# Optimization experiments

Hardware: AMD Instinct MI355X
Metric: run time of the kernel (lower is better)

Reference implementation:

```python
import jax, jax.numpy as jnp
import numpy as np


def _cayley():
    # Cl(3,0) basis blades ordered by grade, lexicographic: 1,e1,e2,e3,e12,e13,e23,e123
    blades = [0b000, 0b001, 0b010, 0b100, 0b011, 0b101, 0b110, 0b111]
    idx = {b: i for i, b in enumerate(blades)}
    C = np.zeros((8, 8, 8), np.float32)
    for a in blades:
        for b in blades:
            t, s = a >> 1, 0
            while t:
                s += bin(t & b).count('1')
                t >>= 1
            C[idx[a], idx[a ^ b], idx[b]] = -1.0 if (s & 1) else 1.0
    return jnp.asarray(C)

CAYLEY = _cayley()                      # [8,8,8], metric [1,1,1]
GRADE = jnp.array([0, 1, 1, 1, 2, 2, 2, 3])  # blade -> grade (subspace) index
N_NODES, N_EDGES = 5, 20
NUM_HEADS = 8


def mv_linear(x, w, b):
    # MVLinear with subspaces=True: one scalar weight per (out, in, grade),
    # expanded to the 8 blades; bias only on the grade-0 (scalar) blade.
    # x: [N, m, 8], w: [n, m, 4], b: [n]
    out = jnp.einsum('bmi,nmi->bni', x, w[:, :, GRADE])
    return out.at[..., 0].add(b)


def _ln(x, g, b):
    m = jnp.mean(x, axis=-1, keepdims=True)
    v = jnp.var(x, axis=-1, keepdims=True)
    return (x - m) * jax.lax.rsqrt(v + 1e-5) * g + b


def _forward(nodes, edges, src_mask, batch_size, W_in, b_in, W_gp, b_gp,
             Wq, Wk, Wv, Wo, ln1_g, ln1_b, ln2_g, ln2_b, W1, b1, W2, b2):
    B = batch_size
    S = N_NODES + N_EDGES
    c_in = nodes.shape[1]
    nodes4 = nodes.reshape(B, N_NODES, c_in, 8)
    edges4 = edges.reshape(B, N_EDGES, c_in, 8)
    src = jnp.concatenate([nodes4, edges4], axis=1).reshape(B * S, c_in, 8)

    src_mv = mv_linear(src, W_in, b_in)                               # [B*S, dm, 8]
    src_gp = jnp.einsum('bni,ijk,bnk->bnj', src_mv, CAYLEY, src_mv)   # geometric product
    src2 = mv_linear(jnp.concatenate([src_mv, src_gp], axis=1), W_gp, b_gp)

    dm = src2.shape[1]
    D = dm * 8                                                        # 56 flat features
    H = NUM_HEADS
    hd = D // H
    x = src2.reshape(B, S, D)

    L = Wq.shape[0]
    for l in range(L):                                                # fixed small layer count
        h = _ln(x, ln1_g[l], ln1_b[l])
        q = (h @ Wq[l]).reshape(B, S, H, hd)
        k = (h @ Wk[l]).reshape(B, S, H, hd)
        v = (h @ Wv[l]).reshape(B, S, H, hd)
        scores = jnp.einsum('bqhd,bkhd->bhqk', q, k) / jnp.sqrt(jnp.float32(hd))
        scores = scores + src_mask[:, None, :, :]
        attn = jax.nn.softmax(scores, axis=-1)
        o = jnp.einsum('bhqk,bkhd->bqhd', attn, v).reshape(B, S, D)
        x = x + o @ Wo[l]
        h2 = _ln(x, ln2_g[l], ln2_b[l])
        x = x + jax.nn.gelu(h2 @ W1[l] + b1[l]) @ W2[l] + b2[l]

    out = x.reshape(B, S, dm, 8)
    sel = out[:, :N_NODES, 1, :]                                      # feature channel 1
    return sel.reshape(B * N_NODES, 8)


def setup_inputs() -> dict:
    key = jax.random.key(0)
    ks = jax.random.split(key, 12)
    B, c_in, dm, L = 4096, 3, 7, 4
    D = dm * 8
    Dff = 4 * D

    def r(k, shp, s=0.02):
        return jax.random.normal(k, shp, jnp.float32) * s

    return dict(
        nodes=jax.random.normal(ks[0], (B * N_NODES, c_in, 8), jnp.float32),
        edges=jax.random.normal(ks[1], (B * N_EDGES, c_in, 8), jnp.float32),
        src_mask=jnp.zeros((B, 25, 25), jnp.float32),
        batch_size=B,
        W_in=r(ks[2], (dm, c_in, 4), 1.0 / np.sqrt(c_in)),
        b_in=jnp.zeros((dm,), jnp.float32),
        W_gp=r(ks[3], (dm, 2 * dm, 4), 1.0 / np.sqrt(2 * dm)),
        b_gp=jnp.zeros((dm,), jnp.float32),
        Wq=r(ks[4], (L, D, D)), Wk=r(ks[5], (L, D, D)),
        Wv=r(ks[6], (L, D, D)), Wo=r(ks[7], (L, D, D)),
        ln1_g=jnp.ones((L, D), jnp.float32), ln1_b=jnp.zeros((L, D), jnp.float32),
        ln2_g=jnp.ones((L, D), jnp.float32), ln2_b=jnp.zeros((L, D), jnp.float32),
        W1=r(ks[8], (L, D, Dff)), b1=jnp.zeros((L, Dff), jnp.float32),
        W2=r(ks[9], (L, Dff, D)), b2=jnp.zeros((L, D), jnp.float32),
    )


def reference(nodes, edges, src_mask, batch_size, W_in, b_in, W_gp, b_gp,
              Wq, Wk, Wv, Wo, ln1_g, ln1_b, ln2_g, ln2_b, W1, b1, W2, b2):
    return _forward(nodes, edges, src_mask, batch_size, W_in, b_in, W_gp, b_gp,
                    Wq, Wk, Wv, Wo, ln1_g, ln1_b, ln2_g, ln2_b, W1, b1, W2, b2)
```

## Files before the change

kernel.cpp:

```cpp
#include <hip/hip_runtime.h>
#include <math.h>

#define NTH 256
#define XSTR 56
#define QHSTR 72
#define FSTR 224
#define LOG2E 1.4426950408889634f

typedef __attribute__((ext_vector_type(8))) short short8;
typedef __attribute__((ext_vector_type(4))) float f32x4;
typedef _Float16 half2_t __attribute__((ext_vector_type(2)));

__device__ __forceinline__ half2_t as_h2(unsigned int u) {
    return __builtin_bit_cast(half2_t, u);
}
__device__ __forceinline__ float fast_exp2(float x) {
    float r;
    asm("v_exp_f32 %0, %1" : "=v"(r) : "v"(x));
    return r;
}
__device__ __forceinline__ unsigned short f2bf(float x) {
    unsigned int u = __float_as_uint(x);
    return (unsigned short)((u + 0x7FFFu + ((u >> 16) & 1u)) >> 16);
}
__device__ __forceinline__ unsigned short f2bf_t(float x) {
    return (unsigned short)(__float_as_uint(x) >> 16);
}

__host__ __device__ constexpr int pc_(int v) { int c = 0; while (v) { c += v & 1; v >>= 1; } return c; }
__host__ __device__ constexpr int gp_sign(int a, int b) {
    int s = 0; int t = a >> 1;
    while (t) { s += pc_(t & b); t >>= 1; }
    return (s & 1) ? -1 : 1;
}
#define BLADE(i) ((int)((0x76534210u >> ((i) * 4)) & 0xF))

__device__ __forceinline__ float gelu_sig(float z) {
    float E = fast_exp2(-2.4554669f * z);
    return z * __builtin_amdgcn_rcpf(1.0f + E);
}

__global__ void prep_weights(const float* __restrict__ Wq, const float* __restrict__ Wk,
                             const float* __restrict__ Wv, const float* __restrict__ Wo,
                             const float* __restrict__ W1, const float* __restrict__ W2,
                             unsigned short* __restrict__ ws, int L)
{
    int idx = blockIdx.x * NTH + threadIdx.x;
    int total1 = L * 16384, total2 = L * 14336, total3 = L * 14336;
    if (idx < total1) {
        int k = idx & 63, n = (idx >> 6) & 63, mat = (idx >> 12) & 3, l = idx >> 14;
        float v = 0.f;
        if (k < 56 && n < 56) {
            const float* W = (mat == 0) ? Wq : (mat == 1) ? Wk : (mat == 2) ? Wv : Wo;
            v = W[l * 3136 + k * 56 + n];
            if (mat == 0) v *= 0.3779644730092272f * LOG2E;
        }
        ws[idx] = f2bf(v);
    } else if (idx < total1 + total2) {
        int t = idx - total1;
        int k = t & 63, n = (t >> 6) % 224, l = t / 14336;
        float v = (k < 56) ? W1[l * 12544 + k * 224 + n] : 0.f;
        ws[idx] = f2bf(v);
    } else if (idx < total1 + total2 + total3) {
        int t = idx - total1 - total2;
        int k = t % 224, n = (t / 224) & 63, l = t / 14336;
        float v = (n < 56) ? W2[l * 12544 + k * 56 + n] : 0.f;
        ws[idx] = f2bf(v);
    }
}

__global__ __launch_bounds__(NTH, 4) void nbody_fused(
    const float* __restrict__ nodes, const float* __restrict__ edges,
    const float* __restrict__ src_mask,
    const float* __restrict__ W_in, const float* __restrict__ b_in,
    const float* __restrict__ W_gp, const float* __restrict__ b_gp,
    const float* __restrict__ ln1g, const float* __restrict__ ln1b,
    const float* __restrict__ ln2g, const float* __restrict__ ln2b,
    const float* __restrict__ b1, const float* __restrict__ b2,
    const unsigned short* __restrict__ ws, int L, int Btot,
    float* __restrict__ out)
{
    __shared__ __align__(16) float XS[2][25 * XSTR];
    __shared__ __align__(16) unsigned short HB[2][1800];
    __shared__ __align__(16) unsigned short UNI[2][5600];

    const int b0 = blockIdx.x * 2, tid = threadIdx.x;
    const int lane = tid & 63, wid = tid >> 6;
    const int nl = lane & 15, quad = lane >> 4;
    const int col = wid * 16 + nl;
    const int pcolh = (col / 7) * 8 + col % 7;
    const int ln_g = lane >> 3, ln_p = lane & 7;
    const int ln_s = wid + 4 * ln_g;
    int rA1 = 16 + nl; if (rA1 > 24) rA1 = 24;
    const int bbm1 = (b0 + 1 < Btot) ? (b0 + 1) : (Btot - 1);

    for (int t = tid; t < 1200; t += NTH) {
        int ss = t / 600, r0 = t - ss * 600;
        int s = r0 / 24, r = r0 % 24;
        int bb = b0 + ss;
        if (bb < Btot)
            XS[ss][r0] = (s < 5) ? nodes[bb * 120 + r0] : edges[bb * 480 + (s - 5) * 24 + r];
    }
    for (int t = tid; t < 400; t += NTH) {
        int ss = t / 200, r0 = t - ss * 200;
        int r = r0 >> 3, c = 56 + (r0 & 7);
        HB[ss][r * 72 + c] = 0;
    }
    __syncthreads();

    #pragma unroll
    for (int ss = 0; ss < 2; ss++) {
        const float* SRCF = XS[ss];
        float* KBs = (float*)UNI[ss];
        for (int t = tid; t < 1400; t += NTH) {
            int s = t / 56, rem = t % 56, n = rem >> 3, i = rem & 7;
            int g = __popc(BLADE(i));
            float acc = (i == 0) ? b_in[n] : 0.0f;
            #pragma unroll
            for (int m = 0; m < 3; m++)
                acc += SRCF[s * 24 + m * 8 + i] * W_in[n * 12 + m * 4 + g];
            KBs[s * 56 + rem] = acc;
        }
    }
    __syncthreads();

    #pragma unroll
    for (int ss = 0; ss < 2; ss++) {
        float* KBs = (float*)UNI[ss];
        float* VBs = KBs + 1400;
        for (int t = tid; t < 175; t += NTH) {
            int s = t / 7, n = t % 7;
            float m8[8], g8[8];
            #pragma unroll
            for (int i = 0; i < 8; i++) { m8[i] = KBs[s * 56 + n * 8 + i]; g8[i] = 0.0f; }
            #pragma unroll
            for (int ai = 0; ai < 8; ai++) {
                const int a = BLADE(ai);
                #pragma unroll
                for (int bi = 0; bi < 8; bi++) {
                    const int bb = BLADE(bi);
                    const int j = BLADE(a ^ bb);
                    const int sg = gp_sign(a, bb);
                    g8[j] += (sg > 0) ? (m8[ai] * m8[bi]) : (-m8[ai] * m8[bi]);
                }
            }
            #pragma unroll
            for (int j = 0; j < 8; j++) VBs[s * 56 + n * 8 + j] = g8[j];
        }
    }
    __syncthreads();

    #pragma unroll
    for (int ss = 0; ss < 2; ss++) {
        const float* KBs = (const float*)UNI[ss];
        const float* VBs = KBs + 1400;
        for (int t = tid; t < 1400; t += NTH) {
            int s = t / 56, rem = t % 56, n = rem >> 3, i = rem & 7;
            int g = __popc(BLADE(i));
            float acc = (i == 0) ? b_gp[n] : 0.0f;
            #pragma unroll
            for (int m = 0; m < 7; m++)
                acc += KBs[s * 56 + m * 8 + i] * W_gp[n * 56 + m * 4 + g];
            #pragma unroll
            for (int m = 0; m < 7; m++)
                acc += VBs[s * 56 + m * 8 + i] * W_gp[n * 56 + (7 + m) * 4 + g];
            XS[ss][s * XSTR + rem] = acc;
        }
    }
    __syncthreads();

    const unsigned short* w1t_all = ws + (size_t)L * 16384;
    const unsigned short* w2t_all = w1t_all + (size_t)L * 14336;

    for (int l = 0; l < L; l++) {
        const float* g1 = ln1g + l * 56; const float* e1 = ln1b + l * 56;
        const float* g2 = ln2g + l * 56; const float* e2 = ln2b + l * 56;

        if (tid < 200) {
            int s = tid >> 3, hh = tid & 7;
            #pragma unroll
            for (int ss = 0; ss < 2; ss++) {
                _Float16* QH = (_Float16*)UNI[ss];
                _Float16* KH = QH + 25 * QHSTR;
                QH[s * QHSTR + hh * 8 + 7] = (_Float16)0.f;
                KH[s * QHSTR + hh * 8 + 7] = (_Float16)0.f;
            }
        }
        #pragma unroll
        for (int ss = 0; ss < 2; ss++) {
            float x[7]; float sum = 0.f, sq = 0.f;
            if (ln_s < 25) {
                const float* xp = XS[ss] + ln_s * XSTR + ln_p * 7;
                #pragma unroll
                for (int j = 0; j < 7; j++) { x[j] = xp[j]; sum += x[j]; sq += x[j] * x[j]; }
            }
            #pragma unroll
            for (int off = 1; off < 8; off <<= 1) {
                sum += __shfl_xor(sum, off, 64);
                sq  += __shfl_xor(sq,  off, 64);
            }
            if (ln_s < 25) {
                float mean = sum * (1.0f / 56.0f);
                float rs = __builtin_amdgcn_rsqf(sq * (1.0f / 56.0f) - mean * mean + 1e-5f);
                unsigned short* hp = HB[ss] + ln_s * 72 + ln_p * 7;
                #pragma unroll
                for (int j = 0; j < 7; j++) {
                    int d = ln_p * 7 + j;
                    hp[j] = f2bf_t((x[j] - mean) * rs * g1[d] + e1[d]);
                }
            }
        }
        __syncthreads();

        {
            short8 a[2][2][2];
            #pragma unroll
            for (int ss = 0; ss < 2; ss++)
                #pragma unroll
                for (int ks = 0; ks < 2; ks++) {
                    a[ss][0][ks] = *(const short8*)(HB[ss] + nl * 72 + ks * 32 + quad * 8);
                    a[ss][1][ks] = *(const short8*)(HB[ss] + rA1 * 72 + ks * 32 + quad * 8);
                }
            #pragma unroll
            for (int mat = 0; mat < 3; mat++) {
                const unsigned short* bp = ws + (((size_t)(l * 4 + mat)) << 12) + (((size_t)col) << 6) + quad * 8;
                short8 b0f = *(const short8*)(bp);
                short8 b1f = *(const short8*)(bp + 32);
                #pragma unroll
                for (int ss = 0; ss < 2; ss++) {
                    f32x4 acc0 = {0, 0, 0, 0}, acc1 = {0, 0, 0, 0};
                    acc0 = __builtin_amdgcn_mfma_f32_16x16x32_bf16(a[ss][0][0], b0f, acc0, 0, 0, 0);
                    acc0 = __builtin_amdgcn_mfma_f32_16x16x32_bf16(a[ss][0][1], b1f, acc0, 0, 0, 0);
                    acc1 = __builtin_amdgcn_mfma_f32_16x16x32_bf16(a[ss][1][0], b0f, acc1, 0, 0, 0);
                    acc1 = __builtin_amdgcn_mfma_f32_16x16x32_bf16(a[ss][1][1], b1f, acc1, 0, 0, 0);
                    _Float16* dst = (_Float16*)UNI[ss] + mat * 25 * QHSTR;
                    if (col < 56) {
                        #pragma unroll
                        for (int r = 0; r < 4; r++) {
                            int row0 = quad * 4 + r;
                            dst[row0 * QHSTR + pcolh] = (_Float16)acc0[r];
                            int row1 = 16 + row0;
                            if (row1 < 25) dst[row1 * QHSTR + pcolh] = (_Float16)acc1[r];
                        }
                    }
                }
            }
        }
        __syncthreads();

        if (tid < 200) {
            int s = tid >> 3, hh = tid & 7;
            const _Float16* QHa = (const _Float16*)UNI[0];
            const _Float16* QHb = (const _Float16*)UNI[1];
            const _Float16* KHa = QHa + 25 * QHSTR, * VHa = KHa + 25 * QHSTR;
            const _Float16* KHb = QHb + 25 * QHSTR, * VHb = KHb + 25 * QHSTR;
            const float* mka = src_mask + (size_t)b0 * 625 + s * 25;
            const float* mkb = src_mask + (size_t)bbm1 * 625 + s * 25;
            uint4 Qa = *(const uint4*)(QHa + s * QHSTR + hh * 8);
            uint4 Qb = *(const uint4*)(QHb + s * QHSTR + hh * 8);
            half2_t qa0 = as_h2(Qa.x), qa1 = as_h2(Qa.y), qa2 = as_h2(Qa.z), qa3 = as_h2(Qa.w);
            half2_t qb0 = as_h2(Qb.x), qb1 = as_h2(Qb.y), qb2 = as_h2(Qb.z), qb3 = as_h2(Qb.w);
            float lsa = 0.f, lsb = 0.f;
            half2_t aa0 = {0,0}, aa1 = {0,0}, aa2 = {0,0}, aa3 = {0,0};
            half2_t ab0 = {0,0}, ab1 = {0,0}, ab2 = {0,0}, ab3 = {0,0};
            for (int kk = 0; kk < 25; kk++) {
                uint4 Ka = *(const uint4*)(KHa + kk * QHSTR + hh * 8);
                uint4 Kb = *(const uint4*)(KHb + kk * QHSTR + hh * 8);
                float da = mka[kk] * LOG2E;
                float db = mkb[kk] * LOG2E;
                da = __builtin_amdgcn_fdot2(qa3, as_h2(Ka.w), da, false);
                db = __builtin_amdgcn_fdot2(qb3, as_h2(Kb.w), db, false);
                da = __builtin_amdgcn_fdot2(qa2, as_h2(Ka.z), da, false);
                db = __builtin_amdgcn_fdot2(qb2, as_h2(Kb.z), db, false);
                da = __builtin_amdgcn_fdot2(qa1, as_h2(Ka.y), da, false);
                db = __builtin_amdgcn_fdot2(qb1, as_h2(Kb.y), db, false);
                da = __builtin_amdgcn_fdot2(qa0, as_h2(Ka.x), da, false);
                db = __builtin_amdgcn_fdot2(qb0, as_h2(Kb.x), db, false);
                float pa = fast_exp2(da);
                float pb = fast_exp2(db);
                lsa += pa; lsb += pb;
                uint4 Va = *(const uint4*)(VHa + kk * QHSTR + hh * 8);
                uint4 Vb = *(const uint4*)(VHb + kk * QHSTR + hh * 8);
                _Float16 pha = (_Float16)pa, phb = (_Float16)pb;
                half2_t p2a = {pha, pha}, p2b = {phb, phb};
                aa0 += p2a * as_h2(Va.x); aa1 += p2a * as_h2(Va.y);
                aa2 += p2a * as_h2(Va.z); aa3 += p2a * as_h2(Va.w);
                ab0 += p2b * as_h2(Vb.x); ab1 += p2b * as_h2(Vb.y);
                ab2 += p2b * as_h2(Vb.z); ab3 += p2b * as_h2(Vb.w);
            }
            float inva = __builtin_amdgcn_rcpf(lsa);
            float invb = __builtin_amdgcn_rcpf(lsb);
            unsigned short* opa = HB[0] + s * 72 + hh * 7;
            unsigned short* opb = HB[1] + s * 72 + hh * 7;
            opa[0] = f2bf_t((float)aa0.x * inva); opa[1] = f2bf_t((float)aa0.y * inva);
            opa[2] = f2bf_t((float)aa1.x * inva); opa[3] = f2bf_t((float)aa1.y * inva);
            opa[4] = f2bf_t((float)aa2.x * inva); opa[5] = f2bf_t((float)aa2.y * inva);
            opa[6] = f2bf_t((float)aa3.x * inva);
            opb[0] = f2bf_t((float)ab0.x * invb); opb[1] = f2bf_t((float)ab0.y * invb);
            opb[2] = f2bf_t((float)ab1.x * invb); opb[3] = f2bf_t((float)ab1.y * invb);
            opb[4] = f2bf_t((float)ab2.x * invb); opb[5] = f2bf_t((float)ab2.y * invb);
            opb[6] = f2bf_t((float)ab3.x * invb);
        }
        __syncthreads();

        {
            short8 a[2][2][2];
            #pragma unroll
            for (int ss = 0; ss < 2; ss++)
                #pragma unroll
                for (int ks = 0; ks < 2; ks++) {
                    a[ss][0][ks] = *(const short8*)(HB[ss] + nl * 72 + ks * 32 + quad * 8);
                    a[ss][1][ks] = *(const short8*)(HB[ss] + rA1 * 72 + ks * 32 + quad * 8);
                }
            const unsigned short* bp = ws + (((size_t)(l * 4 + 3)) << 12) + (((size_t)col) << 6) + quad * 8;
            short8 b0f = *(const short8*)(bp);
            short8 b1f = *(const short8*)(bp + 32);
            #pragma unroll
            for (int ss = 0; ss < 2; ss++) {
                f32x4 acc0 = {0, 0, 0, 0}, acc1 = {0, 0, 0, 0};
                acc0 = __builtin_amdgcn_mfma_f32_16x16x32_bf16(a[ss][0][0], b0f, acc0, 0, 0, 0);
                acc0 = __builtin_amdgcn_mfma_f32_16x16x32_bf16(a[ss][0][1], b1f, acc0, 0, 0, 0);
                acc1 = __builtin_amdgcn_mfma_f32_16x16x32_bf16(a[ss][1][0], b0f, acc1, 0, 0, 0);
                acc1 = __builtin_amdgcn_mfma_f32_16x16x32_bf16(a[ss][1][1], b1f, acc1, 0, 0, 0);
                if (col < 56) {
                    #pragma unroll
                    for (int r = 0; r < 4; r++) {
                        int row0 = quad * 4 + r;
                        XS[ss][row0 * XSTR + col] += acc0[r];
                        int row1 = 16 + row0;
                        if (row1 < 25) XS[ss][row1 * XSTR + col] += acc1[r];
                    }
                }
            }
        }
        __syncthreads();

        #pragma unroll
        for (int ss = 0; ss < 2; ss++) {
            float x[7]; float sum = 0.f, sq = 0.f;
            if (ln_s < 25) {
                const float* xp = XS[ss] + ln_s * XSTR + ln_p * 7;
                #pragma unroll
                for (int j = 0; j < 7; j++) { x[j] = xp[j]; sum += x[j]; sq += x[j] * x[j]; }
            }
            #pragma unroll
            for (int off = 1; off < 8; off <<= 1) {
                sum += __shfl_xor(sum, off, 64);
                sq  += __shfl_xor(sq,  off, 64);
            }
            if (ln_s < 25) {
                float mean = sum * (1.0f / 56.0f);
                float rs = __builtin_amdgcn_rsqf(sq * (1.0f / 56.0f) - mean * mean + 1e-5f);
                unsigned short* hp = HB[ss] + ln_s * 72 + ln_p * 7;
                #pragma unroll
                for (int j = 0; j < 7; j++) {
                    int d = ln_p * 7 + j;
                    hp[j] = f2bf_t((x[j] - mean) * rs * g2[d] + e2[d]);
                }
            }
        }
        __syncthreads();

        {
            short8 a[2][2][2];
            #pragma unroll
            for (int ss = 0; ss < 2; ss++)
                #pragma unroll
                for (int ks = 0; ks < 2; ks++) {
                    a[ss][0][ks] = *(const short8*)(HB[ss] + nl * 72 + ks * 32 + quad * 8);
                    a[ss][1][ks] = *(const short8*)(HB[ss] + rA1 * 72 + ks * 32 + quad * 8);
                }
            for (int u = wid; u < 14; u += 4) {
                int c1 = u * 16 + nl;
                const unsigned short* bp = w1t_all + (((size_t)(l * 224 + c1)) << 6) + quad * 8;
                short8 b0f = *(const short8*)(bp);
                short8 b1f = *(const short8*)(bp + 32);
                float bias = b1[l * 224 + c1];
                #pragma unroll
                for (int ss = 0; ss < 2; ss++) {
                    f32x4 acc0 = {0, 0, 0, 0}, acc1 = {0, 0, 0, 0};
                    acc0 = __builtin_amdgcn_mfma_f32_16x16x32_bf16(a[ss][0][0], b0f, acc0, 0, 0, 0);
                    acc0 = __builtin_amdgcn_mfma_f32_16x16x32_bf16(a[ss][0][1], b1f, acc0, 0, 0, 0);
                    acc1 = __builtin_amdgcn_mfma_f32_16x16x32_bf16(a[ss][1][0], b0f, acc1, 0, 0, 0);
                    acc1 = __builtin_amdgcn_mfma_f32_16x16x32_bf16(a[ss][1][1], b1f, acc1, 0, 0, 0);
                    unsigned short* FB = UNI[ss];
                    #pragma unroll
                    for (int r = 0; r < 4; r++) {
                        int row0 = quad * 4 + r;
                        FB[row0 * FSTR + c1] = f2bf_t(gelu_sig(acc0[r] + bias));
                        int row1 = 16 + row0;
                        if (row1 < 25) FB[row1 * FSTR + c1] = f2bf_t(gelu_sig(acc1[r] + bias));
                    }
                }
            }
        }
        __syncthreads();

        {
            const unsigned short* bp0 = w2t_all + ((size_t)(l * 64 + col)) * 224 + quad * 8;
            f32x4 acc0a = {0,0,0,0}, acc1a = {0,0,0,0}, acc0b = {0,0,0,0}, acc1b = {0,0,0,0};
            #pragma unroll
            for (int ks = 0; ks < 7; ks++) {
                short8 bfrag = *(const short8*)(bp0 + ks * 32);
                const unsigned short* FBa = UNI[0];
                const unsigned short* FBb = UNI[1];
                short8 a0a = *(const short8*)(FBa + nl * FSTR + ks * 32 + quad * 8);
                short8 a1a = *(const short8*)(FBa + rA1 * FSTR + ks * 32 + quad * 8);
                short8 a0b = *(const short8*)(FBb + nl * FSTR + ks * 32 + quad * 8);
                short8 a1b = *(const short8*)(FBb + rA1 * FSTR + ks * 32 + quad * 8);
                acc0a = __builtin_amdgcn_mfma_f32_16x16x32_bf16(a0a, bfrag, acc0a, 0, 0, 0);
                acc0b = __builtin_amdgcn_mfma_f32_16x16x32_bf16(a0b, bfrag, acc0b, 0, 0, 0);
                acc1a = __builtin_amdgcn_mfma_f32_16x16x32_bf16(a1a, bfrag, acc1a, 0, 0, 0);
                acc1b = __builtin_amdgcn_mfma_f32_16x16x32_bf16(a1b, bfrag, acc1b, 0, 0, 0);
            }
            if (col < 56) {
                float bias = b2[l * 56 + col];
                #pragma unroll
                for (int r = 0; r < 4; r++) {
                    int row0 = quad * 4 + r;
                    XS[0][row0 * XSTR + col] += acc0a[r] + bias;
                    XS[1][row0 * XSTR + col] += acc0b[r] + bias;
                    int row1 = 16 + row0;
                    if (row1 < 25) {
                        XS[0][row1 * XSTR + col] += acc1a[r] + bias;
                        XS[1][row1 * XSTR + col] += acc1b[r] + bias;
                    }
                }
            }
        }
        __syncthreads();
    }

    for (int t = tid; t < 80; t += NTH) {
        int ss = t / 40, r = t - ss * 40;
        int s = r >> 3, j = r & 7;
        int bb = b0 + ss;
        if (bb < Btot) out[(bb * 5 + s) * 8 + j] = XS[ss][s * XSTR + 8 + j];
    }
}

extern "C" void kernel_launch(void* const* d_in, const int* in_sizes, int n_in,
                              void* d_out, int out_size, void* d_ws, size_t ws_size,
                              hipStream_t stream) {
    const float* nodes = (const float*)d_in[0];
    const float* edges = (const float*)d_in[1];
    const float* mask  = (const float*)d_in[2];
    const int B = in_sizes[0] / 120;
    const float* W_in = (const float*)d_in[4];
    const float* b_in = (const float*)d_in[5];
    const float* W_gp = (const float*)d_in[6];
    const float* b_gp = (const float*)d_in[7];
    const float* Wq   = (const float*)d_in[8];
    const float* Wk   = (const float*)d_in[9];
    const float* Wv   = (const float*)d_in[10];
    const float* Wo   = (const float*)d_in[11];
    const float* ln1g = (const float*)d_in[12];
    const float* ln1b = (const float*)d_in[13];
    const float* ln2g = (const float*)d_in[14];
    const float* ln2b = (const float*)d_in[15];
    const float* W1   = (const float*)d_in[16];
    const float* b1   = (const float*)d_in[17];
    const float* W2   = (const float*)d_in[18];
    const float* b2   = (const float*)d_in[19];
    float* out = (float*)d_out;
    const int L = in_sizes[8] / 3136;

    unsigned short* ws16 = (unsigned short*)d_ws;
    int prep_total = L * (16384 + 14336 + 14336);
    hipLaunchKernelGGL(prep_weights, dim3((prep_total + NTH - 1) / NTH), dim3(NTH), 0, stream,
                       Wq, Wk, Wv, Wo, W1, W2, ws16, L);

    hipLaunchKernelGGL(nbody_fused, dim3((B + 1) / 2), dim3(NTH), 0, stream,
                       nodes, edges, mask, W_in, b_in, W_gp, b_gp,
                       ln1g, ln1b, ln2g, ln2b, b1, b2, ws16, L, B, out);
}
```

Measured before the change: 293.8 us.

## Shrink LDS footprint with fp16 residual and chunked FFN to raise occupancy

Stores the residual stream in fp16 instead of fp32 and splits the FFN hidden dimension into two 112-wide chunks, so the intermediate buffer and QH stride shrink. W2 is repacked with a 256-wide padded K layout so each chunk can be read separately. Launch bounds go from 4 to 5 blocks per CU to use the freed LDS. This adds a barrier per chunk, and fp16 residual accumulation across layers risks precision loss.

```diff
diff --git a/kernel.cpp b/kernel.cpp
--- a/kernel.cpp
+++ b/kernel.cpp
@@ -2,9 +2,8 @@
 #include <math.h>
 
 #define NTH 256
-#define XSTR 56
-#define QHSTR 72
-#define FSTR 224
+#define QHSTR 64
+#define FSTR 136
 #define LOG2E 1.4426950408889634f
 
 typedef __attribute__((ext_vector_type(8))) short short8;
@@ -46,7 +45,7 @@
                              unsigned short* __restrict__ ws, int L)
 {
     int idx = blockIdx.x * NTH + threadIdx.x;
-    int total1 = L * 16384, total2 = L * 14336, total3 = L * 14336;
+    int total1 = L * 16384, total2 = L * 14336, total3 = L * 16384;
     if (idx < total1) {
         int k = idx & 63, n = (idx >> 6) & 63, mat = (idx >> 12) & 3, l = idx >> 14;
         float v = 0.f;
@@ -63,13 +62,13 @@
         ws[idx] = f2bf(v);
     } else if (idx < total1 + total2 + total3) {
         int t = idx - total1 - total2;
-        int k = t % 224, n = (t / 224) & 63, l = t / 14336;
-        float v = (n < 56) ? W2[l * 12544 + k * 56 + n] : 0.f;
+        int k = t & 255, n = (t >> 8) & 63, l = t >> 14;
+        float v = (k < 224 && n < 56) ? W2[l * 12544 + k * 56 + n] : 0.f;
         ws[idx] = f2bf(v);
     }
 }
 
-__global__ __launch_bounds__(NTH, 4) void nbody_fused(
+__global__ __launch_bounds__(NTH, 5) void nbody_fused(
     const float* __restrict__ nodes, const float* __restrict__ edges,
     const float* __restrict__ src_mask,
     const float* __restrict__ W_in, const float* __restrict__ b_in,
@@ -80,17 +79,17 @@
     const unsigned short* __restrict__ ws, int L, int Btot,
     float* __restrict__ out)
 {
-    __shared__ __align__(16) float XS[2][25 * XSTR];
+    __shared__ __align__(16) _Float16 XSH[2][1400];
     __shared__ __align__(16) unsigned short HB[2][1800];
-    __shared__ __align__(16) unsigned short UNI[2][5600];
+    __shared__ __align__(16) unsigned short UNI[2][4800];
 
     const int b0 = blockIdx.x * 2, tid = threadIdx.x;
     const int lane = tid & 63, wid = tid >> 6;
     const int nl = lane & 15, quad = lane >> 4;
     const int col = wid * 16 + nl;
     const int pcolh = (col / 7) * 8 + col % 7;
-    const int ln_g = lane >> 3, ln_p = lane & 7;
-    const int ln_s = wid + 4 * ln_g;
+    const int ln_p = lane & 7;
+    const int ln_s = wid + 4 * (lane >> 3);
     int rA1 = 16 + nl; if (rA1 > 24) rA1 = 24;
     const int bbm1 = (b0 + 1 < Btot) ? (b0 + 1) : (Btot - 1);
 
@@ -99,7 +98,7 @@
         int s = r0 / 24, r = r0 % 24;
         int bb = b0 + ss;
         if (bb < Btot)
-            XS[ss][r0] = (s < 5) ? nodes[bb * 120 + r0] : edges[bb * 480 + (s - 5) * 24 + r];
+            XSH[ss][r0] = (_Float16)((s < 5) ? nodes[bb * 120 + r0] : edges[bb * 480 + (s - 5) * 24 + r]);
     }
     for (int t = tid; t < 400; t += NTH) {
         int ss = t / 200, r0 = t - ss * 200;
@@ -110,29 +109,28 @@
 
     #pragma unroll
     for (int ss = 0; ss < 2; ss++) {
-        const float* SRCF = XS[ss];
-        float* KBs = (float*)UNI[ss];
+        _Float16* KBs = (_Float16*)UNI[ss];
         for (int t = tid; t < 1400; t += NTH) {
             int s = t / 56, rem = t % 56, n = rem >> 3, i = rem & 7;
             int g = __popc(BLADE(i));
             float acc = (i == 0) ? b_in[n] : 0.0f;
             #pragma unroll
             for (int m = 0; m < 3; m++)
-                acc += SRCF[s * 24 + m * 8 + i] * W_in[n * 12 + m * 4 + g];
-            KBs[s * 56 + rem] = acc;
+                acc += (float)XSH[ss][s * 24 + m * 8 + i] * W_in[n * 12 + m * 4 + g];
+            KBs[s * 56 + rem] = (_Float16)acc;
         }
     }
     __syncthreads();
 
     #pragma unroll
     for (int ss = 0; ss < 2; ss++) {
-        float* KBs = (float*)UNI[ss];
-        float* VBs = KBs + 1400;
+        _Float16* KBs = (_Float16*)UNI[ss];
+        _Float16* VBs = KBs + 1400;
         for (int t = tid; t < 175; t += NTH) {
             int s = t / 7, n = t % 7;
             float m8[8], g8[8];
             #pragma unroll
-            for (int i = 0; i < 8; i++) { m8[i] = KBs[s * 56 + n * 8 + i]; g8[i] = 0.0f; }
+            for (int i = 0; i < 8; i++) { m8[i] = (float)KBs[s * 56 + n * 8 + i]; g8[i] = 0.0f; }
             #pragma unroll
             for (int ai = 0; ai < 8; ai++) {
                 const int a = BLADE(ai);
@@ -145,26 +143,26 @@
                 }
             }
             #pragma unroll
-            for (int j = 0; j < 8; j++) VBs[s * 56 + n * 8 + j] = g8[j];
+            for (int j = 0; j < 8; j++) VBs[s * 56 + n * 8 + j] = (_Float16)g8[j];
         }
     }
     __syncthreads();
 
     #pragma unroll
     for (int ss = 0; ss < 2; ss++) {
-        const float* KBs = (const float*)UNI[ss];
-        const float* VBs = KBs + 1400;
+        const _Float16* KBs = (const _Float16*)UNI[ss];
+        const _Float16* VBs = KBs + 1400;
         for (int t = tid; t < 1400; t += NTH) {
             int s = t / 56, rem = t % 56, n = rem >> 3, i = rem & 7;
             int g = __popc(BLADE(i));
             float acc = (i == 0) ? b_gp[n] : 0.0f;
             #pragma unroll
             for (int m = 0; m < 7; m++)
-                acc += KBs[s * 56 + m * 8 + i] * W_gp[n * 56 + m * 4 + g];
+                acc += (float)KBs[s * 56 + m * 8 + i] * W_gp[n * 56 + m * 4 + g];
             #pragma unroll
             for (int m = 0; m < 7; m++)
-                acc += VBs[s * 56 + m * 8 + i] * W_gp[n * 56 + (7 + m) * 4 + g];
-            XS[ss][s * XSTR + rem] = acc;
+                acc += (float)VBs[s * 56 + m * 8 + i] * W_gp[n * 56 + (7 + m) * 4 + g];
+            XSH[ss][s * 56 + rem] = (_Float16)acc;
         }
     }
     __syncthreads();
@@ -190,9 +188,9 @@
         for (int ss = 0; ss < 2; ss++) {
             float x[7]; float sum = 0.f, sq = 0.f;
             if (ln_s < 25) {
-                const float* xp = XS[ss] + ln_s * XSTR + ln_p * 7;
-                #pragma unroll
-                for (int j = 0; j < 7; j++) { x[j] = xp[j]; sum += x[j]; sq += x[j] * x[j]; }
+                const _Float16* xp = XSH[ss] + ln_s * 56 + ln_p * 7;
+                #pragma unroll
+                for (int j = 0; j < 7; j++) { x[j] = (float)xp[j]; sum += x[j]; sq += x[j] * x[j]; }
             }
             #pragma unroll
             for (int off = 1; off < 8; off <<= 1) {
@@ -326,9 +324,13 @@
                     #pragma unroll
                     for (int r = 0; r < 4; r++) {
                         int row0 = quad * 4 + r;
-                        XS[ss][row0 * XSTR + col] += acc0[r];
+                        _Float16* xp0 = &XSH[ss][row0 * 56 + col];
+                        *xp0 = (_Float16)((float)*xp0 + acc0[r]);
                         int row1 = 16 + row0;
-                        if (row1 < 25) XS[ss][row1 * XSTR + col] += acc1[r];
+                        if (row1 < 25) {
+                            _Float16* xp1 = &XSH[ss][row1 * 56 + col];
+                            *xp1 = (_Float16)((float)*xp1 + acc1[r]);
+                        }
                     }
                 }
             }
@@ -339,9 +341,9 @@
         for (int ss = 0; ss < 2; ss++) {
             float x[7]; float sum = 0.f, sq = 0.f;
             if (ln_s < 25) {
-                const float* xp = XS[ss] + ln_s * XSTR + ln_p * 7;
-                #pragma unroll
-                for (int j = 0; j < 7; j++) { x[j] = xp[j]; sum += x[j]; sq += x[j] * x[j]; }
+                const _Float16* xp = XSH[ss] + ln_s * 56 + ln_p * 7;
+                #pragma unroll
+                for (int j = 0; j < 7; j++) { x[j] = (float)xp[j]; sum += x[j]; sq += x[j] * x[j]; }
             }
             #pragma unroll
             for (int off = 1; off < 8; off <<= 1) {
@@ -370,72 +372,84 @@
                     a[ss][0][ks] = *(const short8*)(HB[ss] + nl * 72 + ks * 32 + quad * 8);
                     a[ss][1][ks] = *(const short8*)(HB[ss] + rA1 * 72 + ks * 32 + quad * 8);
                 }
-            for (int u = wid; u < 14; u += 4) {
-                int c1 = u * 16 + nl;
-                const unsigned short* bp = w1t_all + (((size_t)(l * 224 + c1)) << 6) + quad * 8;
-                short8 b0f = *(const short8*)(bp);
-                short8 b1f = *(const short8*)(bp + 32);
-                float bias = b1[l * 224 + c1];
-                #pragma unroll
-                for (int ss = 0; ss < 2; ss++) {
-                    f32x4 acc0 = {0, 0, 0, 0}, acc1 = {0, 0, 0, 0};
-                    acc0 = __builtin_amdgcn_mfma_f32_16x16x32_bf16(a[ss][0][0], b0f, acc0, 0, 0, 0);
-                    acc0 = __builtin_amdgcn_mfma_f32_16x16x32_bf16(a[ss][0][1], b1f, acc0, 0, 0, 0);
-                    acc1 = __builtin_amdgcn_mfma_f32_16x16x32_bf16(a[ss][1][0], b0f, acc1, 0, 0, 0);
-                    acc1 = __builtin_amdgcn_mfma_f32_16x16x32_bf16(a[ss][1][1], b1f, acc1, 0, 0, 0);
-                    unsigned short* FB = UNI[ss];
+            for (int cc = 0; cc < 2; cc++) {
+                for (int u = wid; u < 7; u += 4) {
+                    int c1 = cc * 112 + u * 16 + nl;
+                    const unsigned short* bp = w1t_all + (((size_t)(l * 224 + c1)) << 6) + quad * 8;
+                    short8 b0f = *(const short8*)(bp);
+                    short8 b1f = *(const short8*)(bp + 32);
+                    float bias = b1[l * 224 + c1];
                     #pragma unroll
-                    for (int r = 0; r < 4; r++) {
-                        int row0 = quad * 4 + r;
-                        FB[row0 * FSTR + c1] = f2bf_t(gelu_sig(acc0[r] + bias));
-                        int row1 = 16 + row0;
-                        if (row1 < 25) FB[row1 * FSTR + c1] = f2bf_t(gelu_sig(acc1[r] + bias));
+                    for (int ss = 0; ss < 2; ss++) {
+                        f32x4 acc0 = {0, 0, 0, 0}, acc1 = {0, 0, 0, 0};
+                        acc0 = __builtin_amdgcn_mfma_f32_16x16x32_bf16(a[ss][0][0], b0f, acc0, 0, 0, 0);
+                        acc0 = __builtin_amdgcn_mfma_f32_16x16x32_bf16(a[ss][0][1], b1f, acc0, 0, 0, 0);
+                        acc1 = __builtin_amdgcn_mfma_f32_16x16x32_bf16(a[ss][1][0], b0f, acc1, 0, 0, 0);
+                        acc1 = __builtin_amdgcn_mfma_f32_16x16x32_bf16(a[ss][1][1], b1f, acc1, 0, 0, 0);
+                        unsigned short* FB = UNI[ss];
+                        int lc = u * 16 + nl;
+                        #pragma unroll
+                        for (int r = 0; r < 4; r++) {
+                            int row0 = quad * 4 + r;
+                            FB[row0 * FSTR + lc] = f2bf_t(gelu_sig(acc0[r] + bias));
+                            int row1 = 16 + row0;
+                            if (row1 < 25) FB[row1 * FSTR + lc] = f2bf_t(gelu_sig(acc1[r] + bias));
+                        }
                     }
                 }
-            }
-        }
-        __syncthreads();
-
-        {
-            const unsigned short* bp0 = w2t_all + ((size_t)(l * 64 + col)) * 224 + quad * 8;
-            f32x4 acc0a = {0,0,0,0}, acc1a = {0,0,0,0}, acc0b = {0,0,0,0}, acc1b = {0,0,0,0};
-            #pragma unroll
-            for (int ks = 0; ks < 7; ks++) {
-                short8 bfrag = *(const short8*)(bp0 + ks * 32);
-                const unsigned short* FBa = UNI[0];
-                const unsigned short* FBb = UNI[1];
-                short8 a0a = *(const short8*)(FBa + nl * FSTR + ks * 32 + quad * 8);
-                short8 a1a = *(const short8*)(FBa + rA1 * FSTR + ks * 32 + quad * 8);
-                short8 a0b = *(const short8*)(FBb + nl * FSTR + ks * 32 + quad * 8);
-                short8 a1b = *(const short8*)(FBb + rA1 * FSTR + ks * 32 + quad * 8);
-                acc0a = __builtin_amdgcn_mfma_f32_16x16x32_bf16(a0a, bfrag, acc0a, 0, 0, 0);
-                acc0b = __builtin_amdgcn_mfma_f32_16x16x32_bf16(a0b, bfrag, acc0b, 0, 0, 0);
-                acc1a = __builtin_amdgcn_mfma_f32_16x16x32_bf16(a1a, bfrag, acc1a, 0, 0, 0);
-                acc1b = __builtin_amdgcn_mfma_f32_16x16x32_bf16(a1b, bfrag, acc1b, 0, 0, 0);
-            }
-            if (col < 56) {
-                float bias = b2[l * 56 + col];
-                #pragma unroll
-                for (int r = 0; r < 4; r++) {
-                    int row0 = quad * 4 + r;
-                    XS[0][row0 * XSTR + col] += acc0a[r] + bias;
-                    XS[1][row0 * XSTR + col] += acc0b[r] + bias;
-                    int row1 = 16 + row0;
-                    if (row1 < 25) {
-                        XS[0][row1 * XSTR + col] += acc1a[r] + bias;
-                        XS[1][row1 * XSTR + col] += acc1b[r] + bias;
+                if (tid < 200) {
+                    int s = tid >> 3, jj = (tid & 7) * 2;
+                    *(unsigned int*)(UNI[0] + s * FSTR + 112 + jj) = 0;
+                    *(unsigned int*)(UNI[1] + s * FSTR + 112 + jj) = 0;
+                }
+                __syncthreads();
+
+                {
+                    const unsigned short* bp0 = w2t_all + (((size_t)(l * 64 + col)) << 8) + cc * 112 + quad * 8;
+                    f32x4 acc0a = {0,0,0,0}, acc1a = {0,0,0,0}, acc0b = {0,0,0,0}, acc1b = {0,0,0,0};
+                    #pragma unroll
+                    for (int ks = 0; ks < 4; ks++) {
+                        short8 bfrag = *(const short8*)(bp0 + ks * 32);
+                        const unsigned short* FBa = UNI[0];
+                        const unsigned short* FBb = UNI[1];
+                        short8 a0a = *(const short8*)(FBa + nl * FSTR + ks * 32 + quad * 8);
+                        short8 a1a = *(const short8*)(FBa + rA1 * FSTR + ks * 32 + quad * 8);
+                        short8 a0b = *(const short8*)(FBb + nl * FSTR + ks * 32 + quad * 8);
+                        short8 a1b = *(const short8*)(FBb + rA1 * FSTR + ks * 32 + quad * 8);
+                        acc0a = __builtin_amdgcn_mfma_f32_16x16x32_bf16(a0a, bfrag, acc0a, 0, 0, 0);
+                        acc0b = __builtin_amdgcn_mfma_f32_16x16x32_bf16(a0b, bfrag, acc0b, 0, 0, 0);
+                        acc1a = __builtin_amdgcn_mfma_f32_16x16x32_bf16(a1a, bfrag, acc1a, 0, 0, 0);
+                        acc1b = __builtin_amdgcn_mfma_f32_16x16x32_bf16(a1b, bfrag, acc1b, 0, 0, 0);
                     }
-                }
-            }
-        }
-        __syncthreads();
+                    if (col < 56) {
+                        float bias = (cc == 0) ? b2[l * 56 + col] : 0.f;
+                        #pragma unroll
+                        for (int r = 0; r < 4; r++) {
+                            int row0 = quad * 4 + r;
+                            _Float16* x0a = &XSH[0][row0 * 56 + col];
+                            _Float16* x0b = &XSH[1][row0 * 56 + col];
+                            *x0a = (_Float16)((float)*x0a + acc0a[r] + bias);
+                            *x0b = (_Float16)((float)*x0b + acc0b[r] + bias);
+                            int row1 = 16 + row0;
+                            if (row1 < 25) {
+                                _Float16* x1a = &XSH[0][row1 * 56 + col];
+                                _Float16* x1b = &XSH[1][row1 * 56 + col];
+                                *x1a = (_Float16)((float)*x1a + acc1a[r] + bias);
+                                *x1b = (_Float16)((float)*x1b + acc1b[r] + bias);
+                            }
+                        }
+                    }
+                }
+                __syncthreads();
+            }
+        }
     }
 
     for (int t = tid; t < 80; t += NTH) {
         int ss = t / 40, r = t - ss * 40;
         int s = r >> 3, j = r & 7;
         int bb = b0 + ss;
-        if (bb < Btot) out[(bb * 5 + s) * 8 + j] = XS[ss][s * XSTR + 8 + j];
+        if (bb < Btot) out[(bb * 5 + s) * 8 + j] = (float)XSH[ss][s * 56 + 8 + j];
     }
 }
 
@@ -466,7 +480,7 @@
     const int L = in_sizes[8] / 3136;
 
     unsigned short* ws16 = (unsigned short*)d_ws;
-    int prep_total = L * (16384 + 14336 + 14336);
+    int prep_total = L * (16384 + 14336 + 16384);
     hipLaunchKernelGGL(prep_weights, dim3((prep_total + NTH - 1) / NTH), dim3(NTH), 0, stream,
                        Wq, Wk, Wv, Wo, W1, W2, ws16, L);
 
```

New measurement: 448.5 us. 52.7% more time.
